# Optimization experiments

Hardware: AMD Instinct MI355X
Metric: run time of the kernel (lower is better)

The kernel has to match this reference:

```python
import jax, jax.numpy as jnp
import numpy as np

NUM_HEADS = 16  # from init_kwargs


def setup_inputs() -> dict:
    key = jax.random.key(0)
    k1, k2, k3, k4, k5 = jax.random.split(key, 5)
    B, N, C = 2, 2048, 1024
    return {
        "query": jax.random.normal(k1, (B, N, C), dtype=jnp.float32),
        "key": jax.random.normal(k2, (B, N, C), dtype=jnp.float32),
        "value": jax.random.normal(k3, (B, N, C), dtype=jnp.float32),
        "W_merge": jax.random.normal(k4, (C, C), dtype=jnp.float32) * (1.0 / np.sqrt(C)),
        "b_merge": jax.random.normal(k5, (C,), dtype=jnp.float32) * 0.02,
    }


def reference(query, key, value, W_merge, b_merge):
    B, N, C = query.shape
    H = NUM_HEADS
    dim = C // H
    # Faithful to torch: plain reshape (B,N,C) -> (B, dim, H, N), no transpose.
    q = query.reshape(B, dim, H, -1)
    k = key.reshape(B, dim, H, -1)
    v = value.reshape(B, dim, H, -1)
    # Faithful scale: divide by sqrt(N) (sequence length), as in the source.
    scale = 1.0 / np.sqrt(N).astype(np.float32)
    scores = jnp.einsum('bdhn,bdhm->bhnm', q, k) * scale  # [B,H,N,N]
    attn = jax.nn.softmax(scores, axis=-1)
    x = jnp.einsum('bhnm,bdhm->bdhn', attn, v)  # [B,dim,H,N]
    x = x.reshape(B, C, -1)  # [B,C,N]
    # Conv1d(C,C,kernel_size=1) == pointwise channel matmul + bias
    out = jnp.einsum('oc,bcn->bon', W_merge, x) + b_merge[None, :, None]
    return out  # [B,C,N]
```

## Files before the change

### kernel.cpp

```cpp
#include <hip/hip_runtime.h>


#define H 16
#define NSEQ 2048
#define CCH 1024
#define BATCH 2
#define DSTR (H * NSEQ)

typedef __attribute__((ext_vector_type(8))) short bf16x8;
typedef __attribute__((ext_vector_type(4))) float f32x4;
typedef __attribute__((ext_vector_type(16))) float f32x16;
typedef __attribute__((ext_vector_type(4))) unsigned int uint32x4;

__device__ __forceinline__ unsigned short f2bf(float x) {
  unsigned int u = __builtin_bit_cast(unsigned int, x);
  u += 0x7FFFu + ((u >> 16) & 1u);
  return (unsigned short)(u >> 16);
}

__device__ __forceinline__ unsigned int pack2bf(float a, float b) {
#if __has_builtin(__builtin_amdgcn_cvt_pk_bf16_f32)
  typedef __attribute__((ext_vector_type(2))) __bf16 bf16x2_t;
  bf16x2_t r = __builtin_amdgcn_cvt_pk_bf16_f32(a, b);
  return __builtin_bit_cast(unsigned int, r);
#else
  unsigned int ua = __builtin_bit_cast(unsigned int, a);
  unsigned int ub = __builtin_bit_cast(unsigned int, b);
  ua += 0x7FFFu + ((ua >> 16) & 1u);
  ub += 0x7FFFu + ((ub >> 16) & 1u);
  return __builtin_amdgcn_perm(ub, ua, 0x07060302u);
#endif
}

__device__ __forceinline__ float fast_exp2(float x) {
#if __has_builtin(__builtin_amdgcn_exp2f)
  return __builtin_amdgcn_exp2f(x);
#else
  return exp2f(x);
#endif
}

__device__ __forceinline__ void permswap32(unsigned int& a, unsigned int& b) {
#if __has_builtin(__builtin_amdgcn_permlane32_swap)
  typedef __attribute__((ext_vector_type(2))) unsigned int uint2v;
  uint2v r = __builtin_amdgcn_permlane32_swap(a, b, false, false);
  a = r[0];
  b = r[1];
#else
  unsigned int ax = (unsigned int)__shfl_xor((int)a, 32, 64);
  unsigned int bx = (unsigned int)__shfl_xor((int)b, 32, 64);
  bool lo = (threadIdx.x & 63) < 32;
  unsigned int na = lo ? a : bx;
  unsigned int nb = lo ? ax : b;
  a = na;
  b = nb;
#endif
}

__device__ __forceinline__ void gld16(const void* g, void* l) {
  __builtin_amdgcn_global_load_lds(
      (const __attribute__((address_space(1))) unsigned int*)g,
      (__attribute__((address_space(3))) unsigned int*)l, 16, 0, 0);
}

__device__ __forceinline__ f32x16 zero16() {
  f32x16 v;
#pragma unroll
  for (int i = 0; i < 16; ++i) v[i] = 0.f;
  return v;
}

__global__ __launch_bounds__(256) void prep_all(const float* __restrict__ W,
                                                const float* __restrict__ v,
                                                const float* __restrict__ q,
                                                const float* __restrict__ k,
                                                unsigned short* __restrict__ Wp,
                                                unsigned short* __restrict__ Vb,
                                                unsigned short* __restrict__ Qt,
                                                unsigned short* __restrict__ Kt) {
  __shared__ unsigned short T[64][72];
  const int bid = blockIdx.x, tid = threadIdx.x;

  if (bid < 1024) {
    const int o = bid;
    const int cp = tid * 4;
    const int hh = cp >> 6;
    const int d0 = cp & 63;
    const float* Wr = W + (size_t)o * CCH;
    ushort4 ov;
    ov.x = f2bf(Wr[(d0 + 0) * H + hh]);
    ov.y = f2bf(Wr[(d0 + 1) * H + hh]);
    ov.z = f2bf(Wr[(d0 + 2) * H + hh]);
    ov.w = f2bf(Wr[(d0 + 3) * H + hh]);
    *(ushort4*)&Wp[(size_t)o * CCH + cp] = ov;
  } else if (bid < 5120) {
    int idx = (bid - 1024) * 256 + tid;
    float4 x = ((const float4*)v)[idx];
    ushort4 o;
    o.x = f2bf(x.x); o.y = f2bf(x.y); o.z = f2bf(x.z); o.w = f2bf(x.w);
    ((ushort4*)Vb)[idx] = o;
  } else {
    const int lbid = bid - 5120;
    const int n0 = (lbid & 31) * 64;
    const int hh = (lbid >> 5) & 15;
    const int zz = lbid >> 9;
    const int b = zz >> 1, t = zz & 1;
    const float* src = t ? k : q;
    unsigned short* dst = t ? Kt : Qt;
    const float scl = t ? 1.0f : (0.022097086912079608f * 1.4426950408889634f);
    const size_t base = (size_t)b * (CCH * NSEQ) + (size_t)hh * NSEQ;
#pragma unroll
    for (int it = 0; it < 4; ++it) {
      int i4 = it * 256 + tid;
      int d = i4 >> 4;
      int nn = (i4 & 15) << 2;
      float4 val = *(const float4*)(src + base + (size_t)d * DSTR + n0 + nn);
      T[nn + 0][d] = f2bf(val.x * scl);
      T[nn + 1][d] = f2bf(val.y * scl);
      T[nn + 2][d] = f2bf(val.z * scl);
      T[nn + 3][d] = f2bf(val.w * scl);
    }
    __syncthreads();
    const size_t obase = ((size_t)(b * H + hh) * NSEQ + n0) * 64;
#pragma unroll
    for (int it = 0; it < 2; ++it) {
      int idx = it * 256 + tid;
      int row = idx >> 3, cb = idx & 7;
      *(bf16x8*)(dst + obase + (size_t)row * 64 + cb * 8) = *(const bf16x8*)&T[row][cb * 8];
    }
  }
}

__global__ __launch_bounds__(256) void attn5(const unsigned short* __restrict__ Qt,
                                             const unsigned short* __restrict__ Kt,
                                             const unsigned short* __restrict__ Vb,
                                             unsigned short* __restrict__ xt) {
  __shared__ __align__(16) unsigned short S[4 * 4096];
#define KS(bb) (S + (bb) * 8192)
#define VS(bb) (S + (bb) * 8192 + 4096)

  const int tid = threadIdx.x;
  const int w = tid >> 6, lane = tid & 63;
  const int lane31 = lane & 31, hl = lane >> 5;
  const int n0 = blockIdx.x * 128;
  const int hh = blockIdx.y, b = blockIdx.z;

  const unsigned short* Qbase = Qt + ((size_t)(b * H + hh) * NSEQ + n0) * 64;
  const unsigned short* Kbase = Kt + ((size_t)(b * H + hh) * NSEQ) * 64;
  const unsigned short* Vbase = Vb + (size_t)b * (CCH * NSEQ) + (size_t)hh * NSEQ;

  const int r8 = lane >> 3, scb = lane & 7;

#pragma unroll
  for (int i = 0; i < 4; ++i) {
    int row = i * 32 + w * 8 + r8;
    int cbl = scb ^ (row & 7);
    gld16(Qbase + (size_t)row * 64 + cbl * 8, S + (i * 32 + w * 8) * 64);
  }
  __syncthreads();

  bf16x8 bQ[4];
#pragma unroll
  for (int ks = 0; ks < 4; ++ks) {
    int row = w * 32 + lane31;
    int phys = (ks * 2 + hl) ^ (row & 7);
    bQ[ks] = *(const bf16x8*)(S + (size_t)row * 64 + phys * 8);
  }
  __syncthreads();

#pragma unroll
  for (int i = 0; i < 2; ++i) {
    int row = i * 32 + w * 8 + r8;
    int cbl = scb ^ (row & 7);
    gld16(Kbase + (size_t)row * 64 + cbl * 8, KS(0) + (i * 32 + w * 8) * 64);
    gld16(Vbase + (size_t)row * DSTR + cbl * 8, VS(0) + (i * 32 + w * 8) * 64);
  }
  __syncthreads();

  f32x16 O[2];
  O[0] = zero16();
  O[1] = zero16();
  float lsum = 0.f;

  for (int it = 0; it < 32; ++it) {
    const int cur = it & 1;
    if (it < 31) {
      const int nxt = cur ^ 1;
      const int m0n = (it + 1) * 64;
#pragma unroll
      for (int i = 0; i < 2; ++i) {
        int row = i * 32 + w * 8 + r8;
        int cbl = scb ^ (row & 7);
        gld16(Kbase + (size_t)(m0n + row) * 64 + cbl * 8, KS(nxt) + (i * 32 + w * 8) * 64);
        gld16(Vbase + (size_t)row * DSTR + m0n + cbl * 8, VS(nxt) + (i * 32 + w * 8) * 64);
      }
    }

#pragma unroll
    for (int mt = 0; mt < 2; ++mt) {
      f32x16 St = zero16();
#pragma unroll
      for (int ks = 0; ks < 4; ++ks) {
        int row = mt * 32 + lane31;
        int phys = (ks * 2 + hl) ^ (row & 7);
        bf16x8 aK = *(const bf16x8*)(KS(cur) + row * 64 + phys * 8);
        St = __builtin_amdgcn_mfma_f32_32x32x16_bf16(aK, bQ[ks], St, 0, 0, 0);
      }

      unsigned int pd[8];
#pragma unroll
      for (int t = 0; t < 8; ++t) {
        float e0 = fast_exp2(St[2 * t]);
        float e1 = fast_exp2(St[2 * t + 1]);
        lsum += e0 + e1;
        pd[t] = pack2bf(e0, e1);
      }

      unsigned int s0[4] = {pd[0], pd[1], pd[2], pd[3]};
      unsigned int s1[4] = {pd[4], pd[5], pd[6], pd[7]};
      permswap32(s0[0], s0[2]);
      permswap32(s0[1], s0[3]);
      permswap32(s1[0], s1[2]);
      permswap32(s1[1], s1[3]);

#pragma unroll
      for (int ms = 0; ms < 2; ++ms) {
        bf16x8 bV[2];
#pragma unroll
        for (int dt = 0; dt < 2; ++dt) {
          int row = dt * 32 + lane31;
          int phys = (mt * 4 + ms * 2 + hl) ^ (row & 7);
          bV[dt] = *(const bf16x8*)(VS(cur) + row * 64 + phys * 8);
        }
        const unsigned int* sp = ms ? s1 : s0;
        bf16x8 aP = __builtin_bit_cast(bf16x8, (uint32x4){sp[0], sp[1], sp[2], sp[3]});
        O[0] = __builtin_amdgcn_mfma_f32_32x32x16_bf16(aP, bV[0], O[0], 0, 0, 0);
        O[1] = __builtin_amdgcn_mfma_f32_32x32x16_bf16(aP, bV[1], O[1], 0, 0, 0);
      }
    }
    __syncthreads();
  }

  lsum += __shfl_xor(lsum, 32, 64);
  float linv = 1.0f / lsum;

  const size_t xb = (size_t)b * ((size_t)NSEQ * CCH);
#pragma unroll
  for (int r = 0; r < 16; ++r) {
    int nl = (r & 3) + 8 * (r >> 2) + 4 * hl;
    float inv = __shfl(linv, nl, 64);
    int n = n0 + w * 32 + nl;
    size_t rowb = xb + (size_t)n * CCH + hh * 64;
    xt[rowb + lane31] = f2bf(O[0][r] * inv);
    xt[rowb + 32 + lane31] = f2bf(O[1][r] * inv);
  }
#undef KS
#undef VS
}

__global__ __launch_bounds__(256) void merge4(const unsigned short* __restrict__ Wp,
                                              const unsigned short* __restrict__ xt,
                                              const float* __restrict__ bias,
                                              float* __restrict__ out) {
  __shared__ unsigned short At[2][64 * 64];
  __shared__ unsigned short Bt[2][128 * 64];
  const int tid = threadIdx.x;
  const int w = tid >> 6, lane = tid & 63;
  const int quad = lane >> 4, l16 = lane & 15;
  const int n0 = blockIdx.x * 128, o0 = blockIdx.y * 64, b = blockIdx.z;
  const int srow = w * 8 + (lane >> 3), scb = lane & 7;
  const unsigned short* Bbase = xt + (size_t)b * ((size_t)NSEQ * CCH);

  f32x4 acc[4][2];
#pragma unroll
  for (int ot = 0; ot < 4; ++ot)
#pragma unroll
    for (int nt = 0; nt < 2; ++nt) acc[ot][nt] = (f32x4){0.f, 0.f, 0.f, 0.f};

#pragma unroll
  for (int i = 0; i < 2; ++i) {
    int row = i * 32 + srow;
    int cbl = scb ^ (row & 7);
    gld16(Wp + (size_t)(o0 + row) * CCH + cbl * 8, &At[0][(i * 32 + w * 8) * 64]);
  }
#pragma unroll
  for (int i = 0; i < 4; ++i) {
    int row = i * 32 + srow;
    int cbl = scb ^ (row & 7);
    gld16(Bbase + (size_t)(n0 + row) * CCH + cbl * 8, &Bt[0][(i * 32 + w * 8) * 64]);
  }
  __syncthreads();

  for (int it = 0; it < 16; ++it) {
    const int cur = it & 1;
    if (it < 15) {
      const int nxt = cur ^ 1;
      const int c0 = (it + 1) * 64;
#pragma unroll
      for (int i = 0; i < 2; ++i) {
        int row = i * 32 + srow;
        int cbl = scb ^ (row & 7);
        gld16(Wp + (size_t)(o0 + row) * CCH + c0 + cbl * 8, &At[nxt][(i * 32 + w * 8) * 64]);
      }
#pragma unroll
      for (int i = 0; i < 4; ++i) {
        int row = i * 32 + srow;
        int cbl = scb ^ (row & 7);
        gld16(Bbase + (size_t)(n0 + row) * CCH + c0 + cbl * 8, &Bt[nxt][(i * 32 + w * 8) * 64]);
      }
    }
#pragma unroll
    for (int ks = 0; ks < 2; ++ks) {
      int phys = ((ks * 4 + quad) ^ (l16 & 7)) * 8;
      bf16x8 aW[4], bX[2];
#pragma unroll
      for (int ot = 0; ot < 4; ++ot)
        aW[ot] = *(const bf16x8*)&At[cur][(ot * 16 + l16) * 64 + phys];
#pragma unroll
      for (int nt = 0; nt < 2; ++nt)
        bX[nt] = *(const bf16x8*)&Bt[cur][(w * 32 + nt * 16 + l16) * 64 + phys];
#pragma unroll
      for (int ot = 0; ot < 4; ++ot)
#pragma unroll
        for (int nt = 0; nt < 2; ++nt)
          acc[ot][nt] =
              __builtin_amdgcn_mfma_f32_16x16x32_bf16(aW[ot], bX[nt], acc[ot][nt], 0, 0, 0);
    }
    __syncthreads();
  }

#pragma unroll
  for (int ot = 0; ot < 4; ++ot) {
    float4 bi = *(const float4*)&bias[o0 + ot * 16 + quad * 4];
#pragma unroll
    for (int r = 0; r < 4; ++r) {
      int o = o0 + ot * 16 + quad * 4 + r;
      float br = (r == 0) ? bi.x : (r == 1) ? bi.y : (r == 2) ? bi.z : bi.w;
#pragma unroll
      for (int nt = 0; nt < 2; ++nt)
        out[(size_t)b * ((size_t)CCH * NSEQ) + (size_t)o * NSEQ + n0 + w * 32 + nt * 16 + l16] =
            acc[ot][nt][r] + br;
    }
  }
}

extern "C" void kernel_launch(void* const* d_in, const int* in_sizes, int n_in,
                              void* d_out, int out_size, void* d_ws, size_t ws_size,
                              hipStream_t stream) {
  const float* q = (const float*)d_in[0];
  const float* k = (const float*)d_in[1];
  const float* v = (const float*)d_in[2];
  const float* W = (const float*)d_in[3];
  const float* bias = (const float*)d_in[4];
  float* out = (float*)d_out;

  unsigned short* Wp = (unsigned short*)d_ws;
  unsigned short* xt = Wp + (1u << 20);
  unsigned short* Qt = xt + (4u << 20);
  unsigned short* Kt = Qt + (4u << 20);
  unsigned short* Vb = Kt + (4u << 20);

  hipLaunchKernelGGL(prep_all, dim3(7168), dim3(256), 0, stream, W, v, q, k, Wp, Vb, Qt, Kt);
  hipLaunchKernelGGL(attn5, dim3(NSEQ / 128, H, BATCH), dim3(256), 0, stream, Qt, Kt, Vb, xt);
  hipLaunchKernelGGL(merge4, dim3(NSEQ / 128, CCH / 64, BATCH), dim3(256), 0, stream,
                     Wp, xt, bias, out);
}
```

Baseline: 171.5 us.

## Split attention KV range across two warp groups and shrink merge GEMM tiles

The attention kernel now runs 512 threads per block: two 4-wave groups each process half of the key/value sequence with their own double-buffered LDS tiles, then combine partial outputs and row sums through LDS before normalizing and writing. This halves the serial loop length per block and doubles wave-level parallelism on the attention stage. The merge GEMM switches to 64x64 output tiles with a 2x2 wave layout, doubling the grid to improve occupancy at the cost of more redundant operand loads. LDS use per attention block grows to about 65KB, which may limit blocks per CU.

```diff
diff --git a/kernel.cpp b/kernel.cpp
--- a/kernel.cpp
+++ b/kernel.cpp
@@ -131,49 +131,53 @@
   }
 }
 
-__global__ __launch_bounds__(256) void attn5(const unsigned short* __restrict__ Qt,
-                                             const unsigned short* __restrict__ Kt,
-                                             const unsigned short* __restrict__ Vb,
-                                             unsigned short* __restrict__ xt) {
-  __shared__ __align__(16) unsigned short S[4 * 4096];
-#define KS(bb) (S + (bb) * 8192)
-#define VS(bb) (S + (bb) * 8192 + 4096)
+__global__ __launch_bounds__(512, 4) void attn6(const unsigned short* __restrict__ Qt,
+                                                const unsigned short* __restrict__ Kt,
+                                                const unsigned short* __restrict__ Vb,
+                                                unsigned short* __restrict__ xt) {
+  __shared__ __align__(16) unsigned char sbuf[65536 + 1024];
+  unsigned short* KV = (unsigned short*)sbuf;
+  float* lsumLDS = (float*)(sbuf + 65536);
+  float* Oex = (float*)sbuf;
 
   const int tid = threadIdx.x;
   const int w = tid >> 6, lane = tid & 63;
   const int lane31 = lane & 31, hl = lane >> 5;
+  const int g = w >> 2, nw = w & 3;
   const int n0 = blockIdx.x * 128;
   const int hh = blockIdx.y, b = blockIdx.z;
 
   const unsigned short* Qbase = Qt + ((size_t)(b * H + hh) * NSEQ + n0) * 64;
-  const unsigned short* Kbase = Kt + ((size_t)(b * H + hh) * NSEQ) * 64;
-  const unsigned short* Vbase = Vb + (size_t)b * (CCH * NSEQ) + (size_t)hh * NSEQ;
+  const unsigned short* Kg = Kt + ((size_t)(b * H + hh) * NSEQ + g * 1024) * 64;
+  const unsigned short* Vg = Vb + (size_t)b * (CCH * NSEQ) + (size_t)hh * NSEQ + g * 1024;
 
   const int r8 = lane >> 3, scb = lane & 7;
 
-#pragma unroll
-  for (int i = 0; i < 4; ++i) {
-    int row = i * 32 + w * 8 + r8;
+#define KVOFF(gg, bb, kk) ((((gg)*2 + (bb)) * 2 + (kk)) * 4096)
+
+#pragma unroll
+  for (int i = 0; i < 2; ++i) {
+    int row = i * 64 + w * 8 + r8;
     int cbl = scb ^ (row & 7);
-    gld16(Qbase + (size_t)row * 64 + cbl * 8, S + (i * 32 + w * 8) * 64);
+    gld16(Qbase + (size_t)row * 64 + cbl * 8, KV + (i * 64 + w * 8) * 64);
   }
   __syncthreads();
 
   bf16x8 bQ[4];
 #pragma unroll
   for (int ks = 0; ks < 4; ++ks) {
-    int row = w * 32 + lane31;
+    int row = nw * 32 + lane31;
     int phys = (ks * 2 + hl) ^ (row & 7);
-    bQ[ks] = *(const bf16x8*)(S + (size_t)row * 64 + phys * 8);
+    bQ[ks] = *(const bf16x8*)(KV + (size_t)row * 64 + phys * 8);
   }
   __syncthreads();
 
 #pragma unroll
   for (int i = 0; i < 2; ++i) {
-    int row = i * 32 + w * 8 + r8;
+    int row = i * 32 + nw * 8 + r8;
     int cbl = scb ^ (row & 7);
-    gld16(Kbase + (size_t)row * 64 + cbl * 8, KS(0) + (i * 32 + w * 8) * 64);
-    gld16(Vbase + (size_t)row * DSTR + cbl * 8, VS(0) + (i * 32 + w * 8) * 64);
+    gld16(Kg + (size_t)row * 64 + cbl * 8, KV + KVOFF(g, 0, 0) + (i * 32 + nw * 8) * 64);
+    gld16(Vg + (size_t)row * DSTR + cbl * 8, KV + KVOFF(g, 0, 1) + (i * 32 + nw * 8) * 64);
   }
   __syncthreads();
 
@@ -182,17 +186,19 @@
   O[1] = zero16();
   float lsum = 0.f;
 
-  for (int it = 0; it < 32; ++it) {
+  for (int it = 0; it < 16; ++it) {
     const int cur = it & 1;
-    if (it < 31) {
+    if (it < 15) {
       const int nxt = cur ^ 1;
       const int m0n = (it + 1) * 64;
 #pragma unroll
       for (int i = 0; i < 2; ++i) {
-        int row = i * 32 + w * 8 + r8;
+        int row = i * 32 + nw * 8 + r8;
         int cbl = scb ^ (row & 7);
-        gld16(Kbase + (size_t)(m0n + row) * 64 + cbl * 8, KS(nxt) + (i * 32 + w * 8) * 64);
-        gld16(Vbase + (size_t)row * DSTR + m0n + cbl * 8, VS(nxt) + (i * 32 + w * 8) * 64);
+        gld16(Kg + (size_t)(m0n + row) * 64 + cbl * 8,
+              KV + KVOFF(g, nxt, 0) + (i * 32 + nw * 8) * 64);
+        gld16(Vg + (size_t)row * DSTR + m0n + cbl * 8,
+              KV + KVOFF(g, nxt, 1) + (i * 32 + nw * 8) * 64);
       }
     }
 
@@ -203,7 +209,7 @@
       for (int ks = 0; ks < 4; ++ks) {
         int row = mt * 32 + lane31;
         int phys = (ks * 2 + hl) ^ (row & 7);
-        bf16x8 aK = *(const bf16x8*)(KS(cur) + row * 64 + phys * 8);
+        bf16x8 aK = *(const bf16x8*)(KV + KVOFF(g, cur, 0) + row * 64 + phys * 8);
         St = __builtin_amdgcn_mfma_f32_32x32x16_bf16(aK, bQ[ks], St, 0, 0, 0);
       }
 
@@ -230,7 +236,7 @@
         for (int dt = 0; dt < 2; ++dt) {
           int row = dt * 32 + lane31;
           int phys = (mt * 4 + ms * 2 + hl) ^ (row & 7);
-          bV[dt] = *(const bf16x8*)(VS(cur) + row * 64 + phys * 8);
+          bV[dt] = *(const bf16x8*)(KV + KVOFF(g, cur, 1) + row * 64 + phys * 8);
         }
         const unsigned int* sp = ms ? s1 : s0;
         bf16x8 aP = __builtin_bit_cast(bf16x8, (uint32x4){sp[0], sp[1], sp[2], sp[3]});
@@ -242,38 +248,62 @@
   }
 
   lsum += __shfl_xor(lsum, 32, 64);
-  float linv = 1.0f / lsum;
-
-  const size_t xb = (size_t)b * ((size_t)NSEQ * CCH);
-#pragma unroll
-  for (int r = 0; r < 16; ++r) {
-    int nl = (r & 3) + 8 * (r >> 2) + 4 * hl;
-    float inv = __shfl(linv, nl, 64);
-    int n = n0 + w * 32 + nl;
-    size_t rowb = xb + (size_t)n * CCH + hh * 64;
-    xt[rowb + lane31] = f2bf(O[0][r] * inv);
-    xt[rowb + 32 + lane31] = f2bf(O[1][r] * inv);
-  }
-#undef KS
-#undef VS
-}
-
-__global__ __launch_bounds__(256) void merge4(const unsigned short* __restrict__ Wp,
+  if (hl == 0) lsumLDS[g * 128 + nw * 32 + lane31] = lsum;
+  if (g == 1) {
+#pragma unroll
+    for (int dt = 0; dt < 2; ++dt)
+#pragma unroll
+      for (int r = 0; r < 16; ++r) {
+        int nl = nw * 32 + (r & 3) + 8 * (r >> 2) + 4 * hl;
+        Oex[nl * 64 + dt * 32 + lane31] = O[dt][r];
+      }
+  }
+  __syncthreads();
+  if (g == 0) {
+    const size_t xb = (size_t)b * ((size_t)NSEQ * CCH);
+#pragma unroll
+    for (int rq = 0; rq < 4; ++rq) {
+      int nlb = nw * 32 + rq * 8 + 4 * hl;
+      float4 l0 = *(const float4*)&lsumLDS[nlb];
+      float4 l1 = *(const float4*)&lsumLDS[128 + nlb];
+      float inv0 = 1.0f / (l0.x + l1.x);
+      float inv1 = 1.0f / (l0.y + l1.y);
+      float inv2 = 1.0f / (l0.z + l1.z);
+      float inv3 = 1.0f / (l0.w + l1.w);
+#pragma unroll
+      for (int dt = 0; dt < 2; ++dt) {
+        int d = dt * 32 + lane31;
+#pragma unroll
+        for (int rr = 0; rr < 4; ++rr) {
+          int r = rq * 4 + rr;
+          float val = O[dt][r] + Oex[(nlb + rr) * 64 + d];
+          float inv = (rr == 0) ? inv0 : (rr == 1) ? inv1 : (rr == 2) ? inv2 : inv3;
+          int n = n0 + nlb + rr;
+          xt[xb + (size_t)n * CCH + hh * 64 + d] = f2bf(val * inv);
+        }
+      }
+    }
+  }
+#undef KVOFF
+}
+
+__global__ __launch_bounds__(256) void merge5(const unsigned short* __restrict__ Wp,
                                               const unsigned short* __restrict__ xt,
                                               const float* __restrict__ bias,
                                               float* __restrict__ out) {
   __shared__ unsigned short At[2][64 * 64];
-  __shared__ unsigned short Bt[2][128 * 64];
+  __shared__ unsigned short Bt[2][64 * 64];
   const int tid = threadIdx.x;
   const int w = tid >> 6, lane = tid & 63;
   const int quad = lane >> 4, l16 = lane & 15;
-  const int n0 = blockIdx.x * 128, o0 = blockIdx.y * 64, b = blockIdx.z;
+  const int wx = w & 1, wy = w >> 1;
+  const int n0 = blockIdx.x * 64, o0 = blockIdx.y * 64, b = blockIdx.z;
   const int srow = w * 8 + (lane >> 3), scb = lane & 7;
   const unsigned short* Bbase = xt + (size_t)b * ((size_t)NSEQ * CCH);
 
-  f32x4 acc[4][2];
-#pragma unroll
-  for (int ot = 0; ot < 4; ++ot)
+  f32x4 acc[2][2];
+#pragma unroll
+  for (int ot = 0; ot < 2; ++ot)
 #pragma unroll
     for (int nt = 0; nt < 2; ++nt) acc[ot][nt] = (f32x4){0.f, 0.f, 0.f, 0.f};
 
@@ -282,11 +312,6 @@
     int row = i * 32 + srow;
     int cbl = scb ^ (row & 7);
     gld16(Wp + (size_t)(o0 + row) * CCH + cbl * 8, &At[0][(i * 32 + w * 8) * 64]);
-  }
-#pragma unroll
-  for (int i = 0; i < 4; ++i) {
-    int row = i * 32 + srow;
-    int cbl = scb ^ (row & 7);
     gld16(Bbase + (size_t)(n0 + row) * CCH + cbl * 8, &Bt[0][(i * 32 + w * 8) * 64]);
   }
   __syncthreads();
@@ -301,26 +326,21 @@
         int row = i * 32 + srow;
         int cbl = scb ^ (row & 7);
         gld16(Wp + (size_t)(o0 + row) * CCH + c0 + cbl * 8, &At[nxt][(i * 32 + w * 8) * 64]);
-      }
-#pragma unroll
-      for (int i = 0; i < 4; ++i) {
-        int row = i * 32 + srow;
-        int cbl = scb ^ (row & 7);
         gld16(Bbase + (size_t)(n0 + row) * CCH + c0 + cbl * 8, &Bt[nxt][(i * 32 + w * 8) * 64]);
       }
     }
 #pragma unroll
     for (int ks = 0; ks < 2; ++ks) {
       int phys = ((ks * 4 + quad) ^ (l16 & 7)) * 8;
-      bf16x8 aW[4], bX[2];
-#pragma unroll
-      for (int ot = 0; ot < 4; ++ot)
-        aW[ot] = *(const bf16x8*)&At[cur][(ot * 16 + l16) * 64 + phys];
+      bf16x8 aW[2], bX[2];
+#pragma unroll
+      for (int ot = 0; ot < 2; ++ot)
+        aW[ot] = *(const bf16x8*)&At[cur][(wy * 32 + ot * 16 + l16) * 64 + phys];
 #pragma unroll
       for (int nt = 0; nt < 2; ++nt)
-        bX[nt] = *(const bf16x8*)&Bt[cur][(w * 32 + nt * 16 + l16) * 64 + phys];
-#pragma unroll
-      for (int ot = 0; ot < 4; ++ot)
+        bX[nt] = *(const bf16x8*)&Bt[cur][(wx * 32 + nt * 16 + l16) * 64 + phys];
+#pragma unroll
+      for (int ot = 0; ot < 2; ++ot)
 #pragma unroll
         for (int nt = 0; nt < 2; ++nt)
           acc[ot][nt] =
@@ -330,15 +350,14 @@
   }
 
 #pragma unroll
-  for (int ot = 0; ot < 4; ++ot) {
-    float4 bi = *(const float4*)&bias[o0 + ot * 16 + quad * 4];
+  for (int ot = 0; ot < 2; ++ot) {
 #pragma unroll
     for (int r = 0; r < 4; ++r) {
-      int o = o0 + ot * 16 + quad * 4 + r;
-      float br = (r == 0) ? bi.x : (r == 1) ? bi.y : (r == 2) ? bi.z : bi.w;
+      int o = o0 + wy * 32 + ot * 16 + quad * 4 + r;
+      float br = bias[o];
 #pragma unroll
       for (int nt = 0; nt < 2; ++nt)
-        out[(size_t)b * ((size_t)CCH * NSEQ) + (size_t)o * NSEQ + n0 + w * 32 + nt * 16 + l16] =
+        out[(size_t)b * ((size_t)CCH * NSEQ) + (size_t)o * NSEQ + n0 + wx * 32 + nt * 16 + l16] =
             acc[ot][nt][r] + br;
     }
   }
@@ -361,7 +380,7 @@
   unsigned short* Vb = Kt + (4u << 20);
 
   hipLaunchKernelGGL(prep_all, dim3(7168), dim3(256), 0, stream, W, v, q, k, Wp, Vb, Qt, Kt);
-  hipLaunchKernelGGL(attn5, dim3(NSEQ / 128, H, BATCH), dim3(256), 0, stream, Qt, Kt, Vb, xt);
-  hipLaunchKernelGGL(merge4, dim3(NSEQ / 128, CCH / 64, BATCH), dim3(256), 0, stream,
+  hipLaunchKernelGGL(attn6, dim3(NSEQ / 128, H, BATCH), dim3(512), 0, stream, Qt, Kt, Vb, xt);
+  hipLaunchKernelGGL(merge5, dim3(NSEQ / 64, CCH / 64, BATCH), dim3(256), 0, stream,
                      Wp, xt, bias, out);
 }
```

Measured after the change: 160.3 us. 6.5% less time.
